# Optimization experiments

Hardware: AMD Instinct MI355X
Metric: run time of the kernel (lower is better)

The kernel has to match this reference:

```python
import jax, jax.numpy as jnp
import numpy as np

N = 50000
E = 800000
F = 64
OUT = 64
K = 3


def setup_inputs() -> dict:
    key = jax.random.key(0)
    k1, k2, k3, k4, k5, k6 = jax.random.split(key, 6)
    x = jax.random.normal(k1, (N, F), dtype=jnp.float32)
    edge_row = jax.random.randint(k2, (E,), 0, N, dtype=jnp.int32)
    edge_col = jax.random.randint(k3, (E,), 0, N, dtype=jnp.int32)
    # positive edge weights (e.g., normalized adjacency values)
    edge_val = jax.random.uniform(k4, (E,), dtype=jnp.float32)
    W = jax.random.normal(k5, (F * (K + 1), OUT), dtype=jnp.float32) / np.sqrt(F * (K + 1))
    b = jax.random.normal(k6, (OUT,), dtype=jnp.float32) * 0.01
    return {"x": x, "edge_row": edge_row, "edge_col": edge_col,
            "edge_val": edge_val, "W": W, "b": b}


def _spmm(edge_row, edge_col, edge_val, h, n):
    # row i of adj @ h : sum over edges (i, j, v) of v * h[j]
    return jax.ops.segment_sum(edge_val[:, None] * h[edge_col], edge_row,
                               num_segments=n)


def reference(x, edge_row, edge_col, edge_val, W, b):
    out = x
    xs = [x]
    for _ in range(K):
        out = _spmm(edge_row, edge_col, edge_val, out, N)
        xs.append(out)
    h = jnp.concatenate(xs, axis=-1)  # [N, F*(K+1)]
    return h @ W + b
```

## Files before the change

kernel.cpp:

```cpp
#include <hip/hip_runtime.h>


#define F 64
#define OUT 64
#define SCAN_ELEMS 1024
#define NPART 8

__global__ __launch_bounds__(256) void count_rows(
    const int* __restrict__ row, int* __restrict__ counts, int E) {
  int e = blockIdx.x * 256 + threadIdx.x;
  if (e < E) atomicAdd(&counts[row[e]], 1);
}

__global__ __launch_bounds__(256) void block_scan(
    const int* __restrict__ counts, int* __restrict__ offsets,
    int* __restrict__ blockSums, int N) {
  __shared__ int s[256];
  int t = threadIdx.x;
  int base = blockIdx.x * SCAN_ELEMS + t * 4;
  int v0 = 0, v1 = 0, v2 = 0, v3 = 0;
  if (base + 3 < N) {
    int4 c = *(const int4*)&counts[base];
    v0 = c.x; v1 = c.y; v2 = c.z; v3 = c.w;
  } else {
    if (base < N)     v0 = counts[base];
    if (base + 1 < N) v1 = counts[base + 1];
    if (base + 2 < N) v2 = counts[base + 2];
  }
  s[t] = v0 + v1 + v2 + v3;
  __syncthreads();
  for (int d = 1; d < 256; d <<= 1) {
    int x = (t >= d) ? s[t - d] : 0;
    __syncthreads();
    s[t] += x;
    __syncthreads();
  }
  int ex = (t == 0) ? 0 : s[t - 1];
  if (t == 255) blockSums[blockIdx.x] = s[255];
  int o0 = ex, o1 = o0 + v0, o2 = o1 + v1, o3 = o2 + v2;
  if (base + 3 < N) {
    *(int4*)&offsets[base] = make_int4(o0, o1, o2, o3);
  } else {
    if (base < N)     offsets[base]     = o0;
    if (base + 1 < N) offsets[base + 1] = o1;
    if (base + 2 < N) offsets[base + 2] = o2;
  }
}

__global__ __launch_bounds__(64) void scan_sums(int* __restrict__ blockSums, int nb) {
  int lane = threadIdx.x;
  if (nb <= 64) {
    int v = (lane < nb) ? blockSums[lane] : 0;
    int incl = v;
    for (int d = 1; d < 64; d <<= 1) {
      int u = __shfl_up(incl, d, 64);
      if (lane >= d) incl += u;
    }
    if (lane < nb) blockSums[lane] = incl - v;
  } else if (lane == 0) {
    int run = 0;
    for (int i = 0; i < nb; ++i) { int c = blockSums[i]; blockSums[i] = run; run += c; }
  }
}

__global__ __launch_bounds__(256) void add_offsets(
    int* __restrict__ offsets, const int* __restrict__ blockSums,
    int* __restrict__ cursor, int N, int E) {
  int i = blockIdx.x * 256 + threadIdx.x;
  if (i < N) {
    int o = offsets[i] + blockSums[i >> 10];
    offsets[i] = o;
    cursor[i] = o;
  }
  if (i == 0) offsets[N] = E;
}

__global__ __launch_bounds__(256) void scatter_part(
    const int* __restrict__ row, const int* __restrict__ col,
    const float* __restrict__ val, int* __restrict__ cursor,
    float2* __restrict__ recs, int E, int rpp) {
  int part = blockIdx.x & (NPART - 1);
  int e = (blockIdx.x >> 3) * 256 + threadIdx.x;
  if (e >= E) return;
  int r = row[e];
  unsigned lo = (unsigned)(part * rpp);
  if ((unsigned)(r - lo) >= (unsigned)rpp) return;
  int p = atomicAdd(&cursor[r], 1);
  recs[p] = make_float2(__int_as_float(col[e]), val[e]);
}

__global__ __launch_bounds__(256) void spmm_g16(
    const int* __restrict__ off, const float2* __restrict__ recs,
    const float* __restrict__ hin, float* __restrict__ hout, int N) {
  int r = (blockIdx.x * 256 + threadIdx.x) >> 4;
  if (r >= N) return;
  int fp = (threadIdx.x & 15) << 2;
  int i = off[r], end = off[r + 1];
  float4 acc = make_float4(0.f, 0.f, 0.f, 0.f);

  for (; i + 4 <= end; i += 4) {
    float2 e0 = recs[i], e1 = recs[i + 1], e2 = recs[i + 2], e3 = recs[i + 3];
    float4 h0 = *(const float4*)&hin[(size_t)__float_as_int(e0.x) * F + fp];
    float4 h1 = *(const float4*)&hin[(size_t)__float_as_int(e1.x) * F + fp];
    float4 h2 = *(const float4*)&hin[(size_t)__float_as_int(e2.x) * F + fp];
    float4 h3 = *(const float4*)&hin[(size_t)__float_as_int(e3.x) * F + fp];
    acc.x = fmaf(e0.y, h0.x, acc.x); acc.y = fmaf(e0.y, h0.y, acc.y);
    acc.z = fmaf(e0.y, h0.z, acc.z); acc.w = fmaf(e0.y, h0.w, acc.w);
    acc.x = fmaf(e1.y, h1.x, acc.x); acc.y = fmaf(e1.y, h1.y, acc.y);
    acc.z = fmaf(e1.y, h1.z, acc.z); acc.w = fmaf(e1.y, h1.w, acc.w);
    acc.x = fmaf(e2.y, h2.x, acc.x); acc.y = fmaf(e2.y, h2.y, acc.y);
    acc.z = fmaf(e2.y, h2.z, acc.z); acc.w = fmaf(e2.y, h2.w, acc.w);
    acc.x = fmaf(e3.y, h3.x, acc.x); acc.y = fmaf(e3.y, h3.y, acc.y);
    acc.z = fmaf(e3.y, h3.z, acc.z); acc.w = fmaf(e3.y, h3.w, acc.w);
  }
  for (; i < end; ++i) {
    float2 e0 = recs[i];
    float4 h0 = *(const float4*)&hin[(size_t)__float_as_int(e0.x) * F + fp];
    acc.x = fmaf(e0.y, h0.x, acc.x); acc.y = fmaf(e0.y, h0.y, acc.y);
    acc.z = fmaf(e0.y, h0.z, acc.z); acc.w = fmaf(e0.y, h0.w, acc.w);
  }
  *(float4*)&hout[(size_t)r * F + fp] = acc;
}

__global__ __launch_bounds__(256) void gemm_fused4_v2(
    const float* __restrict__ h0, const float* __restrict__ h1,
    const float* __restrict__ h2, const float* __restrict__ W,
    const float* __restrict__ bias, float* __restrict__ out, int N) {
  __shared__ float Ws[64 * 64];
  const float* hs[4] = {h0, h1, h2, out};

  int nl = threadIdx.x >> 2;
  int oq = threadIdx.x & 3;
  int og = oq << 4;
  int node = blockIdx.x * 64 + nl;
  int nodec = min(node, N - 1);

  const float4* b4 = (const float4*)bias;
  float4 a0 = b4[oq * 4 + 0];
  float4 a1 = b4[oq * 4 + 1];
  float4 a2 = b4[oq * 4 + 2];
  float4 a3 = b4[oq * 4 + 3];

  for (int s = 0; s < 4; ++s) {
    __syncthreads();
    const float4* Wg = (const float4*)(W + s * 4096);
#pragma unroll
    for (int i = 0; i < 4; ++i)
      ((float4*)Ws)[threadIdx.x + i * 256] = Wg[threadIdx.x + i * 256];
    __syncthreads();

    const float* hrow = hs[s] + (size_t)nodec * F;
#pragma unroll 4
    for (int k4 = 0; k4 < 16; ++k4) {
      float4 h4 = *(const float4*)&hrow[k4 * 4];
#pragma unroll
      for (int j = 0; j < 4; ++j) {
        float hv = (j == 0) ? h4.x : (j == 1) ? h4.y : (j == 2) ? h4.z : h4.w;
        const float4* w4 = (const float4*)&Ws[(k4 * 4 + j) * 64 + og];
        float4 w0 = w4[0], w1 = w4[1], w2 = w4[2], w3 = w4[3];
        a0.x = fmaf(hv, w0.x, a0.x); a0.y = fmaf(hv, w0.y, a0.y);
        a0.z = fmaf(hv, w0.z, a0.z); a0.w = fmaf(hv, w0.w, a0.w);
        a1.x = fmaf(hv, w1.x, a1.x); a1.y = fmaf(hv, w1.y, a1.y);
        a1.z = fmaf(hv, w1.z, a1.z); a1.w = fmaf(hv, w1.w, a1.w);
        a2.x = fmaf(hv, w2.x, a2.x); a2.y = fmaf(hv, w2.y, a2.y);
        a2.z = fmaf(hv, w2.z, a2.z); a2.w = fmaf(hv, w2.w, a2.w);
        a3.x = fmaf(hv, w3.x, a3.x); a3.y = fmaf(hv, w3.y, a3.y);
        a3.z = fmaf(hv, w3.z, a3.z); a3.w = fmaf(hv, w3.w, a3.w);
      }
    }
  }

  if (node < N) {
    float4* o4 = (float4*)&out[(size_t)node * OUT + og];
    o4[0] = a0; o4[1] = a1; o4[2] = a2; o4[3] = a3;
  }
}

extern "C" void kernel_launch(void* const* d_in, const int* in_sizes, int n_in,
                              void* d_out, int out_size, void* d_ws, size_t ws_size,
                              hipStream_t stream) {
  const float* x    = (const float*)d_in[0];
  const int*   erow = (const int*)d_in[1];
  const int*   ecol = (const int*)d_in[2];
  const float* eval = (const float*)d_in[3];
  const float* W    = (const float*)d_in[4];
  const float* b    = (const float*)d_in[5];
  float* out = (float*)d_out;

  int N = in_sizes[0] / F;
  int E = in_sizes[1];
  size_t SZ = (size_t)N * F * sizeof(float);
  int nScanBlocks = (N + SCAN_ELEMS - 1) / SCAN_ELEMS;
  int rpp = (N + NPART - 1) / NPART;

  char* p = (char*)d_ws;
  float*  hA     = (float*)p;  p += SZ;
  float*  hB     = (float*)p;  p += SZ;
  float2* recs   = (float2*)p; p += (size_t)E * sizeof(float2);
  int*    counts = (int*)p;    p += (size_t)N * sizeof(int);
  int*    offs   = (int*)p;    p += (size_t)(N + 1) * sizeof(int);
  int*    cursor = (int*)p;    p += (size_t)N * sizeof(int);
  int*    bsums  = (int*)p;    p += (size_t)nScanBlocks * sizeof(int);

  int egrid = (E + 255) / 256;
  int g16grid = ((size_t)N * 16 + 255) / 256;
  int ggrid = (N + 63) / 64;

  hipMemsetAsync(counts, 0, (size_t)N * sizeof(int), stream);
  count_rows<<<egrid, 256, 0, stream>>>(erow, counts, E);
  block_scan<<<nScanBlocks, 256, 0, stream>>>(counts, offs, bsums, N);
  scan_sums<<<1, 64, 0, stream>>>(bsums, nScanBlocks);
  add_offsets<<<(N + 255) / 256, 256, 0, stream>>>(offs, bsums, cursor, N, E);
  scatter_part<<<egrid * NPART, 256, 0, stream>>>(erow, ecol, eval, cursor, recs, E, rpp);

  spmm_g16<<<g16grid, 256, 0, stream>>>(offs, recs, x, hA, N);
  spmm_g16<<<g16grid, 256, 0, stream>>>(offs, recs, hA, hB, N);
  spmm_g16<<<g16grid, 256, 0, stream>>>(offs, recs, hB, out, N);

  gemm_fused4_v2<<<ggrid, 256, 0, stream>>>(x, hA, hB, W, b, out, N);
}
```

Before: 217.8 us.

## Bucket CSR edges by column block and compute two nodes per GEMM thread

Edge counting and scatter now bucket each row's edges by column block (col >> 13), so within a row the edges are grouped by source-node range. This aims to improve cache locality of the gathered h rows in the SpMM. It costs a scan array several times larger and adds a col read to the count pass, which is now partitioned. The final GEMM gives each thread two nodes with prefetched h vectors to reuse the shared W loads, and the block-sum scan is parallelized across the wavefront for the larger bucket count.

Result: faster. 202.8 us (-6.9%).

```diff
diff --git a/kernel.cpp b/kernel.cpp
--- a/kernel.cpp
+++ b/kernel.cpp
@@ -5,27 +5,33 @@
 #define OUT 64
 #define SCAN_ELEMS 1024
 #define NPART 8
-
-__global__ __launch_bounds__(256) void count_rows(
-    const int* __restrict__ row, int* __restrict__ counts, int E) {
-  int e = blockIdx.x * 256 + threadIdx.x;
-  if (e < E) atomicAdd(&counts[row[e]], 1);
+#define CB_SHIFT 13
+
+__global__ __launch_bounds__(256) void count_part(
+    const int* __restrict__ row, const int* __restrict__ col,
+    int* __restrict__ counts, int E, int rpp, int ncb) {
+  int part = blockIdx.x & (NPART - 1);
+  int e = (blockIdx.x >> 3) * 256 + threadIdx.x;
+  if (e >= E) return;
+  int r = row[e];
+  if ((unsigned)(r - part * rpp) >= (unsigned)rpp) return;
+  atomicAdd(&counts[r * ncb + (col[e] >> CB_SHIFT)], 1);
 }
 
 __global__ __launch_bounds__(256) void block_scan(
     const int* __restrict__ counts, int* __restrict__ offsets,
-    int* __restrict__ blockSums, int N) {
+    int* __restrict__ blockSums, int B) {
   __shared__ int s[256];
   int t = threadIdx.x;
   int base = blockIdx.x * SCAN_ELEMS + t * 4;
   int v0 = 0, v1 = 0, v2 = 0, v3 = 0;
-  if (base + 3 < N) {
+  if (base + 3 < B) {
     int4 c = *(const int4*)&counts[base];
     v0 = c.x; v1 = c.y; v2 = c.z; v3 = c.w;
   } else {
-    if (base < N)     v0 = counts[base];
-    if (base + 1 < N) v1 = counts[base + 1];
-    if (base + 2 < N) v2 = counts[base + 2];
+    if (base < B)     v0 = counts[base];
+    if (base + 1 < B) v1 = counts[base + 1];
+    if (base + 2 < B) v2 = counts[base + 2];
   }
   s[t] = v0 + v1 + v2 + v3;
   __syncthreads();
@@ -38,64 +44,63 @@
   int ex = (t == 0) ? 0 : s[t - 1];
   if (t == 255) blockSums[blockIdx.x] = s[255];
   int o0 = ex, o1 = o0 + v0, o2 = o1 + v1, o3 = o2 + v2;
-  if (base + 3 < N) {
+  if (base + 3 < B) {
     *(int4*)&offsets[base] = make_int4(o0, o1, o2, o3);
   } else {
-    if (base < N)     offsets[base]     = o0;
-    if (base + 1 < N) offsets[base + 1] = o1;
-    if (base + 2 < N) offsets[base + 2] = o2;
-  }
-}
-
-__global__ __launch_bounds__(64) void scan_sums(int* __restrict__ blockSums, int nb) {
+    if (base < B)     offsets[base]     = o0;
+    if (base + 1 < B) offsets[base + 1] = o1;
+    if (base + 2 < B) offsets[base + 2] = o2;
+  }
+}
+
+__global__ __launch_bounds__(64) void scan_sums(int* __restrict__ bs, int nb) {
   int lane = threadIdx.x;
-  if (nb <= 64) {
-    int v = (lane < nb) ? blockSums[lane] : 0;
-    int incl = v;
-    for (int d = 1; d < 64; d <<= 1) {
-      int u = __shfl_up(incl, d, 64);
-      if (lane >= d) incl += u;
-    }
-    if (lane < nb) blockSums[lane] = incl - v;
-  } else if (lane == 0) {
-    int run = 0;
-    for (int i = 0; i < nb; ++i) { int c = blockSums[i]; blockSums[i] = run; run += c; }
-  }
+  int chunk = (nb + 63) / 64;
+  int b = lane * chunk, e = min(b + chunk, nb);
+  int sum = 0;
+  for (int i = b; i < e; ++i) sum += bs[i];
+  int incl = sum;
+  for (int d = 1; d < 64; d <<= 1) {
+    int u = __shfl_up(incl, d, 64);
+    if (lane >= d) incl += u;
+  }
+  int run = incl - sum;
+  for (int i = b; i < e; ++i) { int c = bs[i]; bs[i] = run; run += c; }
 }
 
 __global__ __launch_bounds__(256) void add_offsets(
     int* __restrict__ offsets, const int* __restrict__ blockSums,
-    int* __restrict__ cursor, int N, int E) {
+    int* __restrict__ cursor, int B, int E) {
   int i = blockIdx.x * 256 + threadIdx.x;
-  if (i < N) {
+  if (i < B) {
     int o = offsets[i] + blockSums[i >> 10];
     offsets[i] = o;
     cursor[i] = o;
   }
-  if (i == 0) offsets[N] = E;
+  if (i == 0) offsets[B] = E;
 }
 
 __global__ __launch_bounds__(256) void scatter_part(
     const int* __restrict__ row, const int* __restrict__ col,
     const float* __restrict__ val, int* __restrict__ cursor,
-    float2* __restrict__ recs, int E, int rpp) {
+    float2* __restrict__ recs, int E, int rpp, int ncb) {
   int part = blockIdx.x & (NPART - 1);
   int e = (blockIdx.x >> 3) * 256 + threadIdx.x;
   if (e >= E) return;
   int r = row[e];
-  unsigned lo = (unsigned)(part * rpp);
-  if ((unsigned)(r - lo) >= (unsigned)rpp) return;
-  int p = atomicAdd(&cursor[r], 1);
-  recs[p] = make_float2(__int_as_float(col[e]), val[e]);
+  if ((unsigned)(r - part * rpp) >= (unsigned)rpp) return;
+  int c = col[e];
+  int p = atomicAdd(&cursor[r * ncb + (c >> CB_SHIFT)], 1);
+  recs[p] = make_float2(__int_as_float(c), val[e]);
 }
 
 __global__ __launch_bounds__(256) void spmm_g16(
     const int* __restrict__ off, const float2* __restrict__ recs,
-    const float* __restrict__ hin, float* __restrict__ hout, int N) {
+    const float* __restrict__ hin, float* __restrict__ hout, int N, int ncb) {
   int r = (blockIdx.x * 256 + threadIdx.x) >> 4;
   if (r >= N) return;
   int fp = (threadIdx.x & 15) << 2;
-  int i = off[r], end = off[r + 1];
+  int i = off[r * ncb], end = off[r * ncb + ncb];
   float4 acc = make_float4(0.f, 0.f, 0.f, 0.f);
 
   for (; i + 4 <= end; i += 4) {
@@ -122,57 +127,76 @@
   *(float4*)&hout[(size_t)r * F + fp] = acc;
 }
 
-__global__ __launch_bounds__(256) void gemm_fused4_v2(
+__global__ __launch_bounds__(256) void gemm_fused4_v5(
     const float* __restrict__ h0, const float* __restrict__ h1,
     const float* __restrict__ h2, const float* __restrict__ W,
     const float* __restrict__ bias, float* __restrict__ out, int N) {
   __shared__ float Ws[64 * 64];
   const float* hs[4] = {h0, h1, h2, out};
 
-  int nl = threadIdx.x >> 2;
-  int oq = threadIdx.x & 3;
+  int t = threadIdx.x;
+  int oq = t & 3;
   int og = oq << 4;
-  int node = blockIdx.x * 64 + nl;
-  int nodec = min(node, N - 1);
+  int ns = t >> 2;
+  int node0 = blockIdx.x * 128;
+  int n0 = min(node0 + ns, N - 1);
+  int n1 = min(node0 + ns + 64, N - 1);
 
   const float4* b4 = (const float4*)bias;
-  float4 a0 = b4[oq * 4 + 0];
-  float4 a1 = b4[oq * 4 + 1];
-  float4 a2 = b4[oq * 4 + 2];
-  float4 a3 = b4[oq * 4 + 3];
-
+  float4 acc[2][4];
+#pragma unroll
+  for (int m = 0; m < 4; ++m) { acc[0][m] = b4[oq * 4 + m]; acc[1][m] = acc[0][m]; }
+
+#pragma unroll
   for (int s = 0; s < 4; ++s) {
     __syncthreads();
     const float4* Wg = (const float4*)(W + s * 4096);
 #pragma unroll
-    for (int i = 0; i < 4; ++i)
-      ((float4*)Ws)[threadIdx.x + i * 256] = Wg[threadIdx.x + i * 256];
-    __syncthreads();
-
-    const float* hrow = hs[s] + (size_t)nodec * F;
-#pragma unroll 4
+    for (int i = 0; i < 4; ++i) ((float4*)Ws)[t + i * 256] = Wg[t + i * 256];
+    __syncthreads();
+
+    const float4* hr0 = (const float4*)(hs[s] + (size_t)n0 * F);
+    const float4* hr1 = (const float4*)(hs[s] + (size_t)n1 * F);
+    float4 hc0 = hr0[0], hc1 = hr1[0], hn0, hn1;
+
+#pragma unroll 2
     for (int k4 = 0; k4 < 16; ++k4) {
-      float4 h4 = *(const float4*)&hrow[k4 * 4];
+      if (k4 < 15) { hn0 = hr0[k4 + 1]; hn1 = hr1[k4 + 1]; }
 #pragma unroll
       for (int j = 0; j < 4; ++j) {
-        float hv = (j == 0) ? h4.x : (j == 1) ? h4.y : (j == 2) ? h4.z : h4.w;
         const float4* w4 = (const float4*)&Ws[(k4 * 4 + j) * 64 + og];
         float4 w0 = w4[0], w1 = w4[1], w2 = w4[2], w3 = w4[3];
-        a0.x = fmaf(hv, w0.x, a0.x); a0.y = fmaf(hv, w0.y, a0.y);
-        a0.z = fmaf(hv, w0.z, a0.z); a0.w = fmaf(hv, w0.w, a0.w);
-        a1.x = fmaf(hv, w1.x, a1.x); a1.y = fmaf(hv, w1.y, a1.y);
-        a1.z = fmaf(hv, w1.z, a1.z); a1.w = fmaf(hv, w1.w, a1.w);
-        a2.x = fmaf(hv, w2.x, a2.x); a2.y = fmaf(hv, w2.y, a2.y);
-        a2.z = fmaf(hv, w2.z, a2.z); a2.w = fmaf(hv, w2.w, a2.w);
-        a3.x = fmaf(hv, w3.x, a3.x); a3.y = fmaf(hv, w3.y, a3.y);
-        a3.z = fmaf(hv, w3.z, a3.z); a3.w = fmaf(hv, w3.w, a3.w);
+        float a = (j == 0) ? hc0.x : (j == 1) ? hc0.y : (j == 2) ? hc0.z : hc0.w;
+        float c = (j == 0) ? hc1.x : (j == 1) ? hc1.y : (j == 2) ? hc1.z : hc1.w;
+        acc[0][0].x = fmaf(a, w0.x, acc[0][0].x); acc[0][0].y = fmaf(a, w0.y, acc[0][0].y);
+        acc[0][0].z = fmaf(a, w0.z, acc[0][0].z); acc[0][0].w = fmaf(a, w0.w, acc[0][0].w);
+        acc[0][1].x = fmaf(a, w1.x, acc[0][1].x); acc[0][1].y = fmaf(a, w1.y, acc[0][1].y);
+        acc[0][1].z = fmaf(a, w1.z, acc[0][1].z); acc[0][1].w = fmaf(a, w1.w, acc[0][1].w);
+        acc[0][2].x = fmaf(a, w2.x, acc[0][2].x); acc[0][2].y = fmaf(a, w2.y, acc[0][2].y);
+        acc[0][2].z = fmaf(a, w2.z, acc[0][2].z); acc[0][2].w = fmaf(a, w2.w, acc[0][2].w);
+        acc[0][3].x = fmaf(a, w3.x, acc[0][3].x); acc[0][3].y = fmaf(a, w3.y, acc[0][3].y);
+        acc[0][3].z = fmaf(a, w3.z, acc[0][3].z); acc[0][3].w = fmaf(a, w3.w, acc[0][3].w);
+        acc[1][0].x = fmaf(c, w0.x, acc[1][0].x); acc[1][0].y = fmaf(c, w0.y, acc[1][0].y);
+        acc[1][0].z = fmaf(c, w0.z, acc[1][0].z); acc[1][0].w = fmaf(c, w0.w, acc[1][0].w);
+        acc[1][1].x = fmaf(c, w1.x, acc[1][1].x); acc[1][1].y = fmaf(c, w1.y, acc[1][1].y);
+        acc[1][1].z = fmaf(c, w1.z, acc[1][1].z); acc[1][1].w = fmaf(c, w1.w, acc[1][1].w);
+        acc[1][2].x = fmaf(c, w2.x, acc[1][2].x); acc[1][2].y = fmaf(c, w2.y, acc[1][2].y);
+        acc[1][2].z = fmaf(c, w2.z, acc[1][2].z); acc[1][2].w = fmaf(c, w2.w, acc[1][2].w);
+        acc[1][3].x = fmaf(c, w3.x, acc[1][3].x); acc[1][3].y = fmaf(c, w3.y, acc[1][3].y);
+        acc[1][3].z = fmaf(c, w3.z, acc[1][3].z); acc[1][3].w = fmaf(c, w3.w, acc[1][3].w);
       }
+      if (k4 < 15) { hc0 = hn0; hc1 = hn1; }
     }
   }
 
-  if (node < N) {
-    float4* o4 = (float4*)&out[(size_t)node * OUT + og];
-    o4[0] = a0; o4[1] = a1; o4[2] = a2; o4[3] = a3;
+  int m0 = node0 + ns, m1 = node0 + ns + 64;
+  if (m0 < N) {
+    float4* o4 = (float4*)&out[(size_t)m0 * OUT + og];
+    o4[0] = acc[0][0]; o4[1] = acc[0][1]; o4[2] = acc[0][2]; o4[3] = acc[0][3];
+  }
+  if (m1 < N) {
+    float4* o4 = (float4*)&out[(size_t)m1 * OUT + og];
+    o4[0] = acc[1][0]; o4[1] = acc[1][1]; o4[2] = acc[1][2]; o4[3] = acc[1][3];
   }
 }
 
@@ -190,32 +214,34 @@
   int N = in_sizes[0] / F;
   int E = in_sizes[1];
   size_t SZ = (size_t)N * F * sizeof(float);
-  int nScanBlocks = (N + SCAN_ELEMS - 1) / SCAN_ELEMS;
+  int ncb = ((N - 1) >> CB_SHIFT) + 1;
+  int B = N * ncb;
+  int nScanBlocks = (B + SCAN_ELEMS - 1) / SCAN_ELEMS;
   int rpp = (N + NPART - 1) / NPART;
 
   char* p = (char*)d_ws;
   float*  hA     = (float*)p;  p += SZ;
   float*  hB     = (float*)p;  p += SZ;
   float2* recs   = (float2*)p; p += (size_t)E * sizeof(float2);
-  int*    counts = (int*)p;    p += (size_t)N * sizeof(int);
-  int*    offs   = (int*)p;    p += (size_t)(N + 1) * sizeof(int);
-  int*    cursor = (int*)p;    p += (size_t)N * sizeof(int);
+  int*    counts = (int*)p;    p += (size_t)B * sizeof(int);
+  int*    offs   = (int*)p;    p += (size_t)(B + 1) * sizeof(int);
+  int*    cursor = (int*)p;    p += (size_t)B * sizeof(int);
   int*    bsums  = (int*)p;    p += (size_t)nScanBlocks * sizeof(int);
 
   int egrid = (E + 255) / 256;
   int g16grid = ((size_t)N * 16 + 255) / 256;
-  int ggrid = (N + 63) / 64;
-
-  hipMemsetAsync(counts, 0, (size_t)N * sizeof(int), stream);
-  count_rows<<<egrid, 256, 0, stream>>>(erow, counts, E);
-  block_scan<<<nScanBlocks, 256, 0, stream>>>(counts, offs, bsums, N);
+  int ggrid = (N + 127) / 128;
+
+  hipMemsetAsync(counts, 0, (size_t)B * sizeof(int), stream);
+  count_part<<<egrid * NPART, 256, 0, stream>>>(erow, ecol, counts, E, rpp, ncb);
+  block_scan<<<nScanBlocks, 256, 0, stream>>>(counts, offs, bsums, B);
   scan_sums<<<1, 64, 0, stream>>>(bsums, nScanBlocks);
-  add_offsets<<<(N + 255) / 256, 256, 0, stream>>>(offs, bsums, cursor, N, E);
-  scatter_part<<<egrid * NPART, 256, 0, stream>>>(erow, ecol, eval, cursor, recs, E, rpp);
-
-  spmm_g16<<<g16grid, 256, 0, stream>>>(offs, recs, x, hA, N);
-  spmm_g16<<<g16grid, 256, 0, stream>>>(offs, recs, hA, hB, N);
-  spmm_g16<<<g16grid, 256, 0, stream>>>(offs, recs, hB, out, N);
-
-  gemm_fused4_v2<<<ggrid, 256, 0, stream>>>(x, hA, hB, W, b, out, N);
-}
+  add_offsets<<<(B + 255) / 256, 256, 0, stream>>>(offs, bsums, cursor, B, E);
+  scatter_part<<<egrid * NPART, 256, 0, stream>>>(erow, ecol, eval, cursor, recs, E, rpp, ncb);
+
+  spmm_g16<<<g16grid, 256, 0, stream>>>(offs, recs, x, hA, N, ncb);
+  spmm_g16<<<g16grid, 256, 0, stream>>>(offs, recs, hA, hB, N, ncb);
+  spmm_g16<<<g16grid, 256, 0, stream>>>(offs, recs, hB, out, N, ncb);
+
+  gemm_fused4_v5<<<ggrid, 256, 0, stream>>>(x, hA, hB, W, b, out, N);
+}
```
